# Performance work log

Measured on AMD Instinct MI355X. Metric: run time of the kernel, lower is better.

## Reference

```python
import jax, jax.numpy as jnp
import numpy as np
import itertools

DIM, KEY_DIM, H, ATTN_RATIO = 576, 32, 18, 4
RES = (14, 14)
DV = ATTN_RATIO * KEY_DIM  # 128
DH = DV * H                # 2304
NH_KD = KEY_DIM * H        # 576
LN_EPS = 1e-5


def _build_bias_idxs():
    points = list(itertools.product(range(RES[0]), range(RES[1])))
    N = len(points)
    offsets = {}
    idxs = []
    for p1 in points:
        for p2 in points:
            off = (abs(p1[0] - p2[0]), abs(p1[1] - p2[1]))
            offsets.setdefault(off, len(offsets))
            idxs.append(offsets[off])
    return np.array(idxs, dtype=np.int64).reshape(N, N), len(offsets)


def setup_inputs() -> dict:
    key = jax.random.key(0)
    ks = jax.random.split(key, 8)
    B, N = 128, RES[0] * RES[1]
    idxs_np, n_off = _build_bias_idxs()  # [N,N], 196 offsets
    x = jax.random.normal(ks[0], (B, N, DIM), dtype=jnp.float32)
    ln_g = jnp.ones((DIM,), jnp.float32)
    ln_b = jnp.zeros((DIM,), jnp.float32)
    qkv_w = jax.random.normal(ks[1], (DH + 2 * NH_KD, DIM), jnp.float32) * (DIM ** -0.5)
    qkv_b = jnp.zeros((DH + 2 * NH_KD,), jnp.float32)
    proj_w = jax.random.normal(ks[2], (DIM, DH), jnp.float32) * (DH ** -0.5)
    proj_b = jnp.zeros((DIM,), jnp.float32)
    attn_biases = jax.random.normal(ks[3], (H, n_off), jnp.float32) * 0.02
    bias_idxs = jnp.asarray(idxs_np)
    return {"x": x, "ln_g": ln_g, "ln_b": ln_b, "qkv_w": qkv_w, "qkv_b": qkv_b,
            "proj_w": proj_w, "proj_b": proj_b, "attn_biases": attn_biases,
            "bias_idxs": bias_idxs}


def reference(x, ln_g, ln_b, qkv_w, qkv_b, proj_w, proj_b, attn_biases, bias_idxs):
    B, N, C = x.shape
    scale = KEY_DIM ** -0.5
    # LayerNorm
    mu = jnp.mean(x, axis=-1, keepdims=True)
    var = jnp.mean(jnp.square(x - mu), axis=-1, keepdims=True)
    xn = (x - mu) * jax.lax.rsqrt(var + LN_EPS) * ln_g + ln_b
    # QKV
    qkv = xn @ qkv_w.T + qkv_b                      # [B,N,H*(2*KD+DV)]
    qkv = qkv.reshape(B, N, H, 2 * KEY_DIM + DV)
    q = qkv[..., :KEY_DIM]                          # [B,N,H,KD]
    k = qkv[..., KEY_DIM:2 * KEY_DIM]
    v = qkv[..., 2 * KEY_DIM:]                      # [B,N,H,DV]
    # Scores + gathered relative-position bias
    bias = attn_biases[:, bias_idxs]                # [H,N,N]
    attn = jnp.einsum('bnhk,bmhk->bhnm', q, k) * scale + bias
    attn = jax.nn.softmax(attn, axis=-1)
    out = jnp.einsum('bhnm,bmhd->bnhd', attn, v).reshape(B, N, DH)
    return out @ proj_w.T + proj_b
```

## Files before the change

kernel.cpp:

```cpp
#include <hip/hip_runtime.h>
#include <hip/hip_bf16.h>
#include <cstdint>


typedef uint32_t u32;
typedef unsigned short u16;
using f32x4 = __attribute__((ext_vector_type(4))) float;
using s16x8 = __attribute__((ext_vector_type(8))) short;

#define DEVFN static __device__ __forceinline__

DEVFN u16 f2bf(float f) {
  u32 u = __builtin_bit_cast(u32, f);
  u = (u + 0x7fffu + ((u >> 16) & 1u)) >> 16;
  return (u16)u;
}

DEVFN u32 cvtpk_bf16(float lo, float hi) {
  u32 r;
  asm("v_cvt_pk_bf16_f32 %0, %1, %2" : "=v"(r) : "v"(lo), "v"(hi));
  return r;
}

DEVFN float exp2_fast(float x) {
  float r;
  asm("v_exp_f32 %0, %1" : "=v"(r) : "v"(x));
  return r;
}

DEVFN void gload_lds16(const void* g, void* l) {
  typedef const __attribute__((address_space(1))) uint32_t* gp_t;
  typedef __attribute__((address_space(3))) uint32_t* lp_t;
  __builtin_amdgcn_global_load_lds((gp_t)g, (lp_t)l, 16, 0, 0);
}

__global__ void k_prep(const float* __restrict__ qkv_w, const float* __restrict__ proj_w,
                       const float* __restrict__ biases, const int* __restrict__ idxs,
                       u16* __restrict__ wq, u16* __restrict__ wp,
                       float* __restrict__ bfull, int noff) {
  int bid = blockIdx.x;
  if (bid < 7776) {
    int i = bid * 256 + threadIdx.x;
    if (i < 1990656) wq[i] = f2bf(qkv_w[i]);
  } else if (bid < 7776 + 5760) {
    int i = (bid - 7776) * 256 + threadIdx.x;
    int r = i / 2304, c = i % 2304;
    wp[i] = (r < 576) ? f2bf(proj_w[r * 2304 + c]) : (u16)0;
  } else {
    int i = (bid - 7776 - 5760) * 256 + threadIdx.x;
    int r = i & 3, g = (i >> 2) & 3, q16 = (i >> 4) & 15;
    int t = i >> 8;
    int mt = t % 13, t2 = t / 13;
    int qt = t2 % 13, h = t2 / 13;
    int q = qt * 16 + q16, m = mt * 16 + g * 4 + r;
    float v = -1e30f;
    if (q < 196 && m < 196)
      v = biases[h * noff + idxs[q * 196 + m]] * 1.4426950408889634f;
    bfull[i] = v;
  }
}

__launch_bounds__(256)
__global__ void k_ln(const float* __restrict__ x, const float* __restrict__ g,
                     const float* __restrict__ b, u16* __restrict__ xn) {
  int t = blockIdx.x * 4 + (threadIdx.x >> 6);
  int l = threadIdx.x & 63;
  const float* xt = x + (size_t)t * 576;
  const float4* x4 = (const float4*)xt;
  float4 v0 = x4[l], v1 = x4[64 + l];
  float v2 = xt[512 + l];
  float s = v0.x + v0.y + v0.z + v0.w + v1.x + v1.y + v1.z + v1.w + v2;
  float q = v0.x * v0.x + v0.y * v0.y + v0.z * v0.z + v0.w * v0.w +
            v1.x * v1.x + v1.y * v1.y + v1.z * v1.z + v1.w * v1.w + v2 * v2;
  for (int o = 1; o < 64; o <<= 1) {
    s += __shfl_xor(s, o, 64);
    q += __shfl_xor(q, o, 64);
  }
  float mean = s * (1.f / 576.f);
  float var = q * (1.f / 576.f) - mean * mean;
  float rstd = rsqrtf(var + 1e-5f);
  const float4* g4 = (const float4*)g;
  const float4* b4 = (const float4*)b;
  float4 ga = g4[l], gb = g4[64 + l];
  float4 ba = b4[l], bb = b4[64 + l];
  float gc = g[512 + l], bc = b[512 + l];
  u16* ot = xn + (size_t)t * 576;
  ushort4 o0, o1;
  o0.x = f2bf((v0.x - mean) * rstd * ga.x + ba.x);
  o0.y = f2bf((v0.y - mean) * rstd * ga.y + ba.y);
  o0.z = f2bf((v0.z - mean) * rstd * ga.z + ba.z);
  o0.w = f2bf((v0.w - mean) * rstd * ga.w + ba.w);
  o1.x = f2bf((v1.x - mean) * rstd * gb.x + bb.x);
  o1.y = f2bf((v1.y - mean) * rstd * gb.y + bb.y);
  o1.z = f2bf((v1.z - mean) * rstd * gb.z + bb.z);
  o1.w = f2bf((v1.w - mean) * rstd * gb.w + bb.w);
  ((ushort4*)ot)[l] = o0;
  ((ushort4*)ot)[64 + l] = o1;
  ot[512 + l] = f2bf((v2 - mean) * rstd * gc + bc);
}

template <bool OBF, int AMODE>
__launch_bounds__(512, 2)
__global__ void k_gemm(const u16* __restrict__ A, const u16* __restrict__ Bt,
                       const float* __restrict__ bias, void* __restrict__ C,
                       int K, int nvalid) {
  __shared__ char smem[73728];
  char* AsB0 = smem;
  char* BsB0 = smem + 49152;
  const int tid = threadIdx.x, lane = tid & 63, w = tid >> 6;
  const int wr = w >> 1, wc = w & 1;
  const int l15 = lane & 15, g = lane >> 4;
  const int nwg = gridDim.x * gridDim.y;
  int wgid = blockIdx.x + gridDim.x * blockIdx.y;
  int xcd = wgid & 7, local = wgid >> 3;
  int nq = nwg >> 3, rr = nwg & 7;
  int id2 = ((xcd < rr) ? xcd * (nq + 1) : rr * (nq + 1) + (xcd - rr) * nq) + local;
  const size_t m0 = (size_t)(id2 / gridDim.x) * 256;
  const size_t n0 = (size_t)(id2 % gridDim.x) * 128;
  const int Kb = K * 2;
  const int KbA = (AMODE == 0) ? K * 2 : 6912;
  const char* Ab = (const char*)A + m0 * KbA;
  const char* Bb = (const char*)Bt + n0 * Kb;
  f32x4 acc[4][4] = {};

  auto stage = [&](int buf, int kt) {
    const int abase = (AMODE == 0) ? kt * 2 : ((kt >> 7) * 384 + 128 + ((kt & 127) << 1));
#pragma unroll
    for (int j = 0; j < 2; ++j) {
      int c = j * 512 + tid;
      int r = c >> 2, sp = c & 3;
      int sl = sp ^ ((r >> 1) & 3);
      gload_lds16(Ab + (size_t)r * KbA + abase + sl * 16,
                  AsB0 + buf * 16384 + c * 16);
    }
    {
      int c = tid;
      int r = c >> 2, sp = c & 3;
      int sl = sp ^ ((r >> 1) & 3);
      gload_lds16(Bb + (size_t)r * Kb + kt * 2 + sl * 16,
                  BsB0 + buf * 8192 + c * 16);
    }
  };

  const int NT = K >> 5;
  stage(0, 0);
  stage(1, 32);
  asm volatile("s_waitcnt vmcnt(3)" ::: "memory");
  __builtin_amdgcn_sched_barrier(0);
  __builtin_amdgcn_s_barrier();

  int br = 0, bs = 2;
  for (int t = 0; t < NT; ++t) {
    const char* AsB = AsB0 + br * 16384;
    const char* BsB = BsB0 + br * 8192;
    s16x8 af[4], bfr[4];
#pragma unroll
    for (int i = 0; i < 4; ++i) {
      int ra = wr * 64 + i * 16 + l15;
      af[i] = *(const s16x8*)(AsB + ra * 64 + ((g ^ ((ra >> 1) & 3)) << 4));
      int rb = wc * 64 + i * 16 + l15;
      bfr[i] = *(const s16x8*)(BsB + rb * 64 + ((g ^ ((rb >> 1) & 3)) << 4));
    }
    if (t + 2 < NT) stage(bs, (t + 2) * 32);
#pragma unroll
    for (int mi = 0; mi < 4; ++mi)
#pragma unroll
      for (int ni = 0; ni < 4; ++ni)
        acc[mi][ni] = __builtin_amdgcn_mfma_f32_16x16x32_bf16(af[mi], bfr[ni], acc[mi][ni], 0, 0, 0);
    if (t + 1 < NT) {
      if (t + 2 < NT) {
        asm volatile("s_waitcnt vmcnt(3)" ::: "memory");
      } else {
        asm volatile("s_waitcnt vmcnt(0)" ::: "memory");
      }
      __builtin_amdgcn_sched_barrier(0);
      __builtin_amdgcn_s_barrier();
    }
    br = (br == 2) ? 0 : br + 1;
    bs = (bs == 2) ? 0 : bs + 1;
  }

  __syncthreads();
  if (OBF) {
    u16* Cs = (u16*)smem;
#pragma unroll
    for (int ni = 0; ni < 4; ++ni) {
      int n_loc = wc * 64 + ni * 16 + l15;
      float bv = bias[n0 + n_loc];
#pragma unroll
      for (int mi = 0; mi < 4; ++mi) {
        int m_base = wr * 64 + mi * 16 + g * 4;
#pragma unroll
        for (int r = 0; r < 4; ++r)
          Cs[(m_base + r) * 128 + n_loc] = f2bf(acc[mi][ni][r] + bv);
      }
    }
    __syncthreads();
    u16* Cg = (u16*)C + m0 * (size_t)nvalid + n0;
#pragma unroll
    for (int i = 0; i < 8; ++i) {
      int c = i * 512 + tid;
      int row = c >> 4, col8 = (c & 15) * 8;
      s16x8 v = *(const s16x8*)(Cs + row * 128 + col8);
      *(s16x8*)(Cg + (size_t)row * nvalid + col8) = v;
    }
  } else {
    float* Cs = (float*)smem;
#pragma unroll
    for (int h = 0; h < 2; ++h) {
      if (wc == h) {
#pragma unroll
        for (int ni = 0; ni < 4; ++ni) {
          int n_loc = ni * 16 + l15;
          int n_glob = (int)n0 + h * 64 + n_loc;
          float bv = (n_glob < nvalid) ? bias[n_glob] : 0.f;
#pragma unroll
          for (int mi = 0; mi < 4; ++mi) {
            int m_base = wr * 64 + mi * 16 + g * 4;
#pragma unroll
            for (int r = 0; r < 4; ++r)
              Cs[(m_base + r) * 64 + n_loc] = acc[mi][ni][r] + bv;
          }
        }
      }
      __syncthreads();
#pragma unroll
      for (int i = 0; i < 8; ++i) {
        int c = i * 512 + tid;
        int row = c >> 4, col4 = (c & 15) * 4;
        int n_glob = (int)n0 + h * 64 + col4;
        if (n_glob < nvalid) {
          float4 v = *(const float4*)(Cs + row * 64 + col4);
          *(float4*)((float*)C + (size_t)(m0 + row) * nvalid + n_glob) = v;
        }
      }
      if (h == 0) __syncthreads();
    }
  }
}

__launch_bounds__(448, 2)
__global__ void k_attn(u16* __restrict__ qkv, const float* __restrict__ biasf) {
  constexpr int LDV = 234;
  __shared__ u16 Vl[128 * LDV];
  __shared__ u16 Kl[13 * 64 * 8];
  const int h = blockIdx.x, b = blockIdx.y;
  const int tid = threadIdx.x, lane = tid & 63, w = tid >> 6;
  const int g = lane >> 4, q16 = lane & 15;
  const size_t tok0 = (size_t)b * 196;
  u16* qkvb = qkv + tok0 * 3456 + (size_t)h * 192;

  {
    int c = tid;
    int tok = min((c >> 6) * 16 + (c & 15), 195);
    gload_lds16(qkvb + (size_t)tok * 3456 + 32 + ((c >> 4) & 3) * 8,
                (char*)Kl + (size_t)(w * 64) * 16);
    if (tid < 384) {
      int c2 = 448 + tid;
      int tok2 = min((c2 >> 6) * 16 + (c2 & 15), 195);
      gload_lds16(qkvb + (size_t)tok2 * 3456 + 32 + ((c2 >> 4) & 3) * 8,
                  (char*)Kl + (size_t)(448 + w * 64) * 16);
    }
  }
  {
    int l15 = lane & 15, g2 = lane >> 4;
    for (int j = w; j < 56; j += 7) {
      int db = j / 14, mb = j % 14;
      int m = mb * 16 + l15, d8 = db * 4 + g2;
      int mc = min(m, 195);
      s16x8 v = *(const s16x8*)(qkvb + (size_t)mc * 3456 + 64 + d8 * 8);
#pragma unroll
      for (int e = 0; e < 8; ++e) Vl[(d8 * 8 + e) * LDV + m] = (u16)v[e];
    }
  }
  __syncthreads();

  const float scale = 0.17677669529663687f * 1.4426950408889634f;
  for (int qt = w; qt < 13; qt += 7) {
    int q = qt * 16 + q16;
    s16x8 qf = *(const s16x8*)(qkvb + (size_t)min(q, 195) * 3456 + g * 8);
    const float* bq = biasf + (((size_t)(h * 13 + qt) * 13) << 8) + (q16 << 4) + (g << 2);
    f32x4 acc[8] = {};
    float sum = 0.f;
    const int L1 = ((g & 1) << 5) + q16;
    const int L2 = L1 + 16;
    const bool hiSel = (g >> 1) != 0;
#pragma unroll
    for (int kk = 0; kk < 7; ++kk) {
      u32 a0, a1, b0 = 0u, b1 = 0u;
      {
        s16x8 kf = *(const s16x8*)(Kl + ((size_t)(2 * kk) * 64 + lane) * 8);
        f32x4 z = {};
        f32x4 t = __builtin_amdgcn_mfma_f32_16x16x32_bf16(kf, qf, z, 0, 0, 0);
        f32x4 b4 = *(const f32x4*)(bq + (2 * kk) * 256);
        float e0 = exp2_fast(t[0] * scale + b4[0]);
        float e1 = exp2_fast(t[1] * scale + b4[1]);
        float e2 = exp2_fast(t[2] * scale + b4[2]);
        float e3 = exp2_fast(t[3] * scale + b4[3]);
        sum += (e0 + e1) + (e2 + e3);
        a0 = cvtpk_bf16(e0, e1);
        a1 = cvtpk_bf16(e2, e3);
      }
      if (2 * kk + 1 < 13) {
        s16x8 kf = *(const s16x8*)(Kl + ((size_t)(2 * kk + 1) * 64 + lane) * 8);
        f32x4 z = {};
        f32x4 t = __builtin_amdgcn_mfma_f32_16x16x32_bf16(kf, qf, z, 0, 0, 0);
        f32x4 b4 = *(const f32x4*)(bq + (2 * kk + 1) * 256);
        float e0 = exp2_fast(t[0] * scale + b4[0]);
        float e1 = exp2_fast(t[1] * scale + b4[1]);
        float e2 = exp2_fast(t[2] * scale + b4[2]);
        float e3 = exp2_fast(t[3] * scale + b4[3]);
        sum += (e0 + e1) + (e2 + e3);
        b0 = cvtpk_bf16(e0, e1);
        b1 = cvtpk_bf16(e2, e3);
      }
      u32 rA0 = __shfl((int)a0, L1, 64), rA1 = __shfl((int)a1, L1, 64);
      u32 rA2 = __shfl((int)a0, L2, 64), rA3 = __shfl((int)a1, L2, 64);
      u32 rB0 = __shfl((int)b0, L1, 64), rB1 = __shfl((int)b1, L1, 64);
      u32 rB2 = __shfl((int)b0, L2, 64), rB3 = __shfl((int)b1, L2, 64);
      union {
        u32 u[4];
        s16x8 v;
      } pa;
      pa.u[0] = hiSel ? rB0 : rA0;
      pa.u[1] = hiSel ? rB1 : rA1;
      pa.u[2] = hiSel ? rB2 : rA2;
      pa.u[3] = hiSel ? rB3 : rA3;
#pragma unroll
      for (int dt = 0; dt < 8; ++dt) {
        s16x8 vf = *(const s16x8*)(Vl + (size_t)(dt * 16 + q16) * LDV + kk * 32 + g * 8);
        acc[dt] = __builtin_amdgcn_mfma_f32_16x16x32_bf16(pa.v, vf, acc[dt], 0, 0, 0);
      }
    }
    sum += __shfl_xor(sum, 16, 64);
    sum += __shfl_xor(sum, 32, 64);
    float inv[4];
#pragma unroll
    for (int r = 0; r < 4; ++r) inv[r] = 1.f / __shfl(sum, g * 4 + r, 64);
#pragma unroll
    for (int dp = 0; dp < 4; ++dp) {
#pragma unroll
      for (int r = 0; r < 4; ++r) {
        int qq = qt * 16 + g * 4 + r;
        if (qq < 196) {
          u32 pk = cvtpk_bf16(acc[2 * dp][r] * inv[r], acc[2 * dp + 1][r] * inv[r]);
          u16* op = qkvb + (size_t)qq * 3456 + 64 + dp * 32 + q16;
          op[0] = (u16)pk;
          op[16] = (u16)(pk >> 16);
        }
      }
    }
  }
}

extern "C" void kernel_launch(void* const* d_in, const int* in_sizes, int n_in,
                              void* d_out, int out_size, void* d_ws, size_t ws_size,
                              hipStream_t stream) {
  const float* x = (const float*)d_in[0];
  const float* ln_g = (const float*)d_in[1];
  const float* ln_b = (const float*)d_in[2];
  const float* qkv_w = (const float*)d_in[3];
  const float* qkv_b = (const float*)d_in[4];
  const float* proj_w = (const float*)d_in[5];
  const float* proj_b = (const float*)d_in[6];
  const float* attnb = (const float*)d_in[7];
  const int* idxs = (const int*)d_in[8];
  const int noff = in_sizes[7] / 18;

  char* ws = (char*)d_ws;
  u16* qkv = (u16*)(ws);
  u16* wq = (u16*)(ws + 173408256);
  u16* wp = (u16*)(ws + 177389568);
  float* bfull = (float*)(ws + 180338688);
  const size_t need = 183453696;
  if (ws_size < need) return;

  u16* xn = (u16*)d_out;
  float* out = (float*)d_out;

  k_prep<<<16578, 256, 0, stream>>>(qkv_w, proj_w, attnb, idxs, wq, wp, bfull, noff);
  k_ln<<<6272, 256, 0, stream>>>(x, ln_g, ln_b, xn);
  k_gemm<true, 0><<<dim3(27, 98), 512, 0, stream>>>(xn, wq, qkv_b, qkv, 576, 3456);
  k_attn<<<dim3(18, 128), 448, 0, stream>>>(qkv, bfull);
  k_gemm<false, 1><<<dim3(5, 98), 512, 0, stream>>>(qkv, wp, proj_b, out, 2304, 576);
}
```

Measured before the change: 343.2 us.

## Process two query tiles per wave in attention and raise MFMA priority

The attention loop is restructured so each wave handles both of its query tiles at once, sharing the K and V fragment loads from LDS across two accumulators instead of looping over tiles sequentially. Waves with only one valid tile compute a duplicate tile and skip storing it. s_setprio is also raised around the MFMA blocks in the GEMM and the PV product to favour matrix issue. This increases register pressure from the doubled accumulators, which could lower occupancy, and waves with a single valid tile now do redundant work.

Result: faster. 331.6 us (-3.4%).

```diff
diff --git a/kernel.cpp b/kernel.cpp
--- a/kernel.cpp
+++ b/kernel.cpp
@@ -162,11 +162,13 @@
       bfr[i] = *(const s16x8*)(BsB + rb * 64 + ((g ^ ((rb >> 1) & 3)) << 4));
     }
     if (t + 2 < NT) stage(bs, (t + 2) * 32);
+    __builtin_amdgcn_s_setprio(1);
 #pragma unroll
     for (int mi = 0; mi < 4; ++mi)
 #pragma unroll
       for (int ni = 0; ni < 4; ++ni)
         acc[mi][ni] = __builtin_amdgcn_mfma_f32_16x16x32_bf16(af[mi], bfr[ni], acc[mi][ni], 0, 0, 0);
+    __builtin_amdgcn_s_setprio(0);
     if (t + 1 < NT) {
       if (t + 2 < NT) {
         asm volatile("s_waitcnt vmcnt(3)" ::: "memory");
@@ -276,75 +278,109 @@
   __syncthreads();
 
   const float scale = 0.17677669529663687f * 1.4426950408889634f;
-  for (int qt = w; qt < 13; qt += 7) {
-    int q = qt * 16 + q16;
-    s16x8 qf = *(const s16x8*)(qkvb + (size_t)min(q, 195) * 3456 + g * 8);
-    const float* bq = biasf + (((size_t)(h * 13 + qt) * 13) << 8) + (q16 << 4) + (g << 2);
-    f32x4 acc[8] = {};
-    float sum = 0.f;
-    const int L1 = ((g & 1) << 5) + q16;
-    const int L2 = L1 + 16;
-    const bool hiSel = (g >> 1) != 0;
-#pragma unroll
-    for (int kk = 0; kk < 7; ++kk) {
+  const int qt0 = w;
+  const bool t1v = (w + 7) < 13;
+  const int qt1 = t1v ? (w + 7) : 12;
+  int q0 = qt0 * 16 + q16, q1 = qt1 * 16 + q16;
+  s16x8 qf0 = *(const s16x8*)(qkvb + (size_t)min(q0, 195) * 3456 + g * 8);
+  s16x8 qf1 = *(const s16x8*)(qkvb + (size_t)min(q1, 195) * 3456 + g * 8);
+  const float* bq0 = biasf + (((size_t)(h * 13 + qt0) * 13) << 8) + (q16 << 4) + (g << 2);
+  const float* bq1 = biasf + (((size_t)(h * 13 + qt1) * 13) << 8) + (q16 << 4) + (g << 2);
+  f32x4 acc0[8] = {}, acc1[8] = {};
+  float sum0 = 0.f, sum1 = 0.f;
+  const int L1 = ((g & 1) << 5) + q16;
+  const int L2 = L1 + 16;
+  const bool hiSel = (g >> 1) != 0;
+
+#pragma unroll
+  for (int kk = 0; kk < 7; ++kk) {
+    const bool hasB = (2 * kk + 1) < 13;
+    s16x8 kfA = *(const s16x8*)(Kl + ((size_t)(2 * kk) * 64 + lane) * 8);
+    s16x8 kfB = {};
+    if (hasB) kfB = *(const s16x8*)(Kl + ((size_t)(2 * kk + 1) * 64 + lane) * 8);
+    u32 pw[2][4];
+#pragma unroll
+    for (int tl = 0; tl < 2; ++tl) {
+      const s16x8 qf = tl ? qf1 : qf0;
+      const float* bq = tl ? bq1 : bq0;
+      float lsum = 0.f;
       u32 a0, a1, b0 = 0u, b1 = 0u;
       {
-        s16x8 kf = *(const s16x8*)(Kl + ((size_t)(2 * kk) * 64 + lane) * 8);
         f32x4 z = {};
-        f32x4 t = __builtin_amdgcn_mfma_f32_16x16x32_bf16(kf, qf, z, 0, 0, 0);
+        f32x4 t = __builtin_amdgcn_mfma_f32_16x16x32_bf16(kfA, qf, z, 0, 0, 0);
         f32x4 b4 = *(const f32x4*)(bq + (2 * kk) * 256);
         float e0 = exp2_fast(t[0] * scale + b4[0]);
         float e1 = exp2_fast(t[1] * scale + b4[1]);
         float e2 = exp2_fast(t[2] * scale + b4[2]);
         float e3 = exp2_fast(t[3] * scale + b4[3]);
-        sum += (e0 + e1) + (e2 + e3);
+        lsum += (e0 + e1) + (e2 + e3);
         a0 = cvtpk_bf16(e0, e1);
         a1 = cvtpk_bf16(e2, e3);
       }
-      if (2 * kk + 1 < 13) {
-        s16x8 kf = *(const s16x8*)(Kl + ((size_t)(2 * kk + 1) * 64 + lane) * 8);
+      if (hasB) {
         f32x4 z = {};
-        f32x4 t = __builtin_amdgcn_mfma_f32_16x16x32_bf16(kf, qf, z, 0, 0, 0);
+        f32x4 t = __builtin_amdgcn_mfma_f32_16x16x32_bf16(kfB, qf, z, 0, 0, 0);
         f32x4 b4 = *(const f32x4*)(bq + (2 * kk + 1) * 256);
         float e0 = exp2_fast(t[0] * scale + b4[0]);
         float e1 = exp2_fast(t[1] * scale + b4[1]);
         float e2 = exp2_fast(t[2] * scale + b4[2]);
         float e3 = exp2_fast(t[3] * scale + b4[3]);
-        sum += (e0 + e1) + (e2 + e3);
+        lsum += (e0 + e1) + (e2 + e3);
         b0 = cvtpk_bf16(e0, e1);
         b1 = cvtpk_bf16(e2, e3);
       }
+      if (tl) sum1 += lsum; else sum0 += lsum;
       u32 rA0 = __shfl((int)a0, L1, 64), rA1 = __shfl((int)a1, L1, 64);
       u32 rA2 = __shfl((int)a0, L2, 64), rA3 = __shfl((int)a1, L2, 64);
       u32 rB0 = __shfl((int)b0, L1, 64), rB1 = __shfl((int)b1, L1, 64);
       u32 rB2 = __shfl((int)b0, L2, 64), rB3 = __shfl((int)b1, L2, 64);
-      union {
-        u32 u[4];
-        s16x8 v;
-      } pa;
-      pa.u[0] = hiSel ? rB0 : rA0;
-      pa.u[1] = hiSel ? rB1 : rA1;
-      pa.u[2] = hiSel ? rB2 : rA2;
-      pa.u[3] = hiSel ? rB3 : rA3;
-#pragma unroll
-      for (int dt = 0; dt < 8; ++dt) {
-        s16x8 vf = *(const s16x8*)(Vl + (size_t)(dt * 16 + q16) * LDV + kk * 32 + g * 8);
-        acc[dt] = __builtin_amdgcn_mfma_f32_16x16x32_bf16(pa.v, vf, acc[dt], 0, 0, 0);
-      }
-    }
-    sum += __shfl_xor(sum, 16, 64);
-    sum += __shfl_xor(sum, 32, 64);
-    float inv[4];
-#pragma unroll
-    for (int r = 0; r < 4; ++r) inv[r] = 1.f / __shfl(sum, g * 4 + r, 64);
-#pragma unroll
-    for (int dp = 0; dp < 4; ++dp) {
-#pragma unroll
-      for (int r = 0; r < 4; ++r) {
-        int qq = qt * 16 + g * 4 + r;
-        if (qq < 196) {
-          u32 pk = cvtpk_bf16(acc[2 * dp][r] * inv[r], acc[2 * dp + 1][r] * inv[r]);
-          u16* op = qkvb + (size_t)qq * 3456 + 64 + dp * 32 + q16;
+      pw[tl][0] = hiSel ? rB0 : rA0;
+      pw[tl][1] = hiSel ? rB1 : rA1;
+      pw[tl][2] = hiSel ? rB2 : rA2;
+      pw[tl][3] = hiSel ? rB3 : rA3;
+    }
+    union {
+      u32 u[4];
+      s16x8 v;
+    } pa0, pa1;
+    pa0.u[0] = pw[0][0]; pa0.u[1] = pw[0][1]; pa0.u[2] = pw[0][2]; pa0.u[3] = pw[0][3];
+    pa1.u[0] = pw[1][0]; pa1.u[1] = pw[1][1]; pa1.u[2] = pw[1][2]; pa1.u[3] = pw[1][3];
+    __builtin_amdgcn_s_setprio(1);
+#pragma unroll
+    for (int dt = 0; dt < 8; ++dt) {
+      s16x8 vf = *(const s16x8*)(Vl + (size_t)(dt * 16 + q16) * LDV + kk * 32 + g * 8);
+      acc0[dt] = __builtin_amdgcn_mfma_f32_16x16x32_bf16(pa0.v, vf, acc0[dt], 0, 0, 0);
+      acc1[dt] = __builtin_amdgcn_mfma_f32_16x16x32_bf16(pa1.v, vf, acc1[dt], 0, 0, 0);
+    }
+    __builtin_amdgcn_s_setprio(0);
+  }
+
+  sum0 += __shfl_xor(sum0, 16, 64);
+  sum0 += __shfl_xor(sum0, 32, 64);
+  sum1 += __shfl_xor(sum1, 16, 64);
+  sum1 += __shfl_xor(sum1, 32, 64);
+  float inv0[4], inv1[4];
+#pragma unroll
+  for (int r = 0; r < 4; ++r) {
+    inv0[r] = 1.f / __shfl(sum0, g * 4 + r, 64);
+    inv1[r] = 1.f / __shfl(sum1, g * 4 + r, 64);
+  }
+#pragma unroll
+  for (int dp = 0; dp < 4; ++dp) {
+#pragma unroll
+    for (int r = 0; r < 4; ++r) {
+      int qq0 = qt0 * 16 + g * 4 + r;
+      if (qq0 < 196) {
+        u32 pk = cvtpk_bf16(acc0[2 * dp][r] * inv0[r], acc0[2 * dp + 1][r] * inv0[r]);
+        u16* op = qkvb + (size_t)qq0 * 3456 + 64 + dp * 32 + q16;
+        op[0] = (u16)pk;
+        op[16] = (u16)(pk >> 16);
+      }
+      if (t1v) {
+        int qq1 = qt1 * 16 + g * 4 + r;
+        if (qq1 < 196) {
+          u32 pk = cvtpk_bf16(acc1[2 * dp][r] * inv1[r], acc1[2 * dp + 1][r] * inv1[r]);
+          u16* op = qkvb + (size_t)qq1 * 3456 + 64 + dp * 32 + q16;
           op[0] = (u16)pk;
           op[16] = (u16)(pk >> 16);
         }
```
